# Performance work log

Measured on AMD Instinct MI355X. Metric: run time of the kernel, lower is better.

The kernel has to match this reference:

```python
import jax, jax.numpy as jnp
import numpy as np

B, F, D = 16384, 40, 32

def setup_inputs() -> dict:
    key = jax.random.key(0)
    k1, k2, k3, k4 = jax.random.split(key, 4)
    g = jax.random.uniform(k1, (B, F, F), dtype=jnp.float32)
    h = jax.random.normal(k2, (B, F, D), dtype=jnp.float32)
    # Xavier-normal init for per-field [D,D] weights: std = sqrt(2/(D+D))
    std = float(np.sqrt(2.0 / (D + D)))
    W_in = jax.random.normal(k3, (F, D, D), dtype=jnp.float32) * std
    W_out = jax.random.normal(k4, (F, D, D), dtype=jnp.float32) * std
    bias_p = jnp.zeros((D,), dtype=jnp.float32)
    return {"g": g, "h": h, "W_in": W_in, "W_out": W_out, "bias_p": bias_p}

def reference(g, h, W_in, W_out, bias_p):
    # per-field transform: [F,D,D] x [B,F,D] -> [B,F,D]
    h_out = jnp.einsum('fde,bfe->bfd', W_out, h)
    # graph aggregation over fields: [B,F,F] x [B,F,D] -> [B,F,D]
    aggr = jnp.einsum('bfg,bgd->bfd', g, h_out)
    # per-field transform + bias
    a = jnp.einsum('fde,bfe->bfd', W_in, aggr) + bias_p
    return a
```

## Files before the change

### kernel.cpp

```cpp
#include <hip/hip_runtime.h>


#define B_TOT 16384
#define FF    40
#define DD    32
#define NB    8
#define WF    10

__global__ __launch_bounds__(256, 4)
void graph_layer_fused(const float* __restrict__ g,
                       const float* __restrict__ h,
                       const float* __restrict__ Win,
                       const float* __restrict__ Wout,
                       const float* __restrict__ bias,
                       float* __restrict__ out)
{
    __shared__ __attribute__((aligned(16))) float s_buf[NB * FF * DD];

    const int t     = threadIdx.x;
    const int w     = t >> 6;
    const int l     = t & 63;
    const int b0    = blockIdx.x * NB;
    const int fbase = w * WF;

    {
        const float4* src = (const float4*)(h + (size_t)b0 * (FF * DD));
        float4* dst = (float4*)s_buf;
        #pragma unroll
        for (int k = 0; k < 10; ++k)
            dst[t + k * 256] = src[t + k * 256];
    }
    __syncthreads();

    const int d    = l & 31;
    const int half = l >> 5;
    float accA[WF][4];
    #pragma unroll
    for (int fi = 0; fi < WF; ++fi) {
        const int f = fbase + fi;
        const float4* wrow = (const float4*)(Wout + ((size_t)f * DD + d) * DD);
        float4 wr[8];
        #pragma unroll
        for (int j = 0; j < 8; ++j) wr[j] = wrow[j];
        #pragma unroll
        for (int bp = 0; bp < 4; ++bp) {
            const int bl = 2 * bp + half;
            const float4* hrow = (const float4*)(s_buf + (bl * FF + f) * DD);
            float p0 = 0.f, p1 = 0.f, p2 = 0.f, p3 = 0.f;
            #pragma unroll
            for (int j = 0; j < 8; ++j) {
                float4 hv = hrow[j];
                p0 += wr[j].x * hv.x; p1 += wr[j].y * hv.y;
                p2 += wr[j].z * hv.z; p3 += wr[j].w * hv.w;
            }
            accA[fi][bp] = (p0 + p1) + (p2 + p3);
        }
    }
    __syncthreads();
    #pragma unroll
    for (int fi = 0; fi < WF; ++fi)
        #pragma unroll
        for (int bp = 0; bp < 4; ++bp) {
            const int bl = 2 * bp + half;
            s_buf[(fbase + fi) * (NB * DD) + bl * DD + d] = accA[fi][bp];
        }
    __syncthreads();

    const int bl = l >> 3;
    const int dq = l & 7;
    const float* grow = g + (size_t)(b0 + bl) * (FF * FF) + (size_t)fbase * FF;
    const float* sb   = s_buf + l * 4;

    float4 accB[WF];
    float4 gv[WF];
    #pragma unroll
    for (int fi = 0; fi < WF; ++fi) {
        accB[fi] = make_float4(0.f, 0.f, 0.f, 0.f);
        gv[fi]   = *(const float4*)(grow + fi * FF);
    }
    #pragma unroll 1
    for (int gc = 0; gc < 10; ++gc) {
        float4 hv[4];
        #pragma unroll
        for (int i = 0; i < 4; ++i)
            hv[i] = *(const float4*)(sb + (4 * gc + i) * (NB * DD));
        const int gnx = (gc < 9) ? 4 * gc + 4 : 36;
        #pragma unroll
        for (int fi = 0; fi < WF; ++fi) {
            float4 gf = gv[fi];
            accB[fi].x += gf.x*hv[0].x + gf.y*hv[1].x + gf.z*hv[2].x + gf.w*hv[3].x;
            accB[fi].y += gf.x*hv[0].y + gf.y*hv[1].y + gf.z*hv[2].y + gf.w*hv[3].y;
            accB[fi].z += gf.x*hv[0].z + gf.y*hv[1].z + gf.z*hv[2].z + gf.w*hv[3].z;
            accB[fi].w += gf.x*hv[0].w + gf.y*hv[1].w + gf.z*hv[2].w + gf.w*hv[3].w;
            gv[fi] = *(const float4*)(grow + fi * FF + gnx);
        }
    }
    __syncthreads();
    #pragma unroll
    for (int fi = 0; fi < WF; ++fi)
        *(float4*)(s_buf + (fbase + fi) * (NB * DD) + bl * DD + dq * 4) = accB[fi];
    __syncthreads();

    {
        const float bv = bias[d];
        #pragma unroll
        for (int fi = 0; fi < WF; ++fi) {
            const int f = fbase + fi;
            const float4* wrow = (const float4*)(Win + ((size_t)f * DD + d) * DD);
            float4 wr[8];
            #pragma unroll
            for (int j = 0; j < 8; ++j) wr[j] = wrow[j];
            #pragma unroll
            for (int bp = 0; bp < 4; ++bp) {
                const int bl2 = 2 * bp + half;
                const float4* arow = (const float4*)(s_buf + f * (NB * DD) + bl2 * DD);
                float p0 = 0.f, p1 = 0.f, p2 = 0.f, p3 = 0.f;
                #pragma unroll
                for (int j = 0; j < 8; ++j) {
                    float4 av = arow[j];
                    p0 += wr[j].x * av.x; p1 += wr[j].y * av.y;
                    p2 += wr[j].z * av.z; p3 += wr[j].w * av.w;
                }
                out[((size_t)(b0 + bl2) * FF + f) * DD + d] =
                    ((p0 + p1) + (p2 + p3)) + bv;
            }
        }
    }
}

extern "C" void kernel_launch(void* const* d_in, const int* in_sizes, int n_in,
                              void* d_out, int out_size, void* d_ws, size_t ws_size,
                              hipStream_t stream) {
    const float* g    = (const float*)d_in[0];
    const float* h    = (const float*)d_in[1];
    const float* Win  = (const float*)d_in[2];
    const float* Wout = (const float*)d_in[3];
    const float* bias = (const float*)d_in[4];
    float* out = (float*)d_out;

    dim3 block(256);
    dim3 grid(B_TOT / NB);
    graph_layer_fused<<<grid, block, 0, stream>>>(g, h, Win, Wout, bias, out);
}
```

Baseline: 374.4 us.

## Halve batch tile, write stage results in place, drop barriers

Each block now processes 4 batch rows instead of 8, which halves LDS use and doubles the launch-bounds occupancy target. The per-field transform writes its results back in place in the [b][f][d] layout, so the separate register accumulator and transposed store pass go away along with one barrier. The aggregation stage's thread mapping changes so each wave only produces the fields it later consumes, which lets a per-wave s_waitcnt stand in for the final __syncthreads. The risk is that smaller tiles reload the weights and g rows more often per batch row, and that the correctness now depends on same-wave ordering of LDS accesses.

```diff
diff --git a/kernel.cpp b/kernel.cpp
--- a/kernel.cpp
+++ b/kernel.cpp
@@ -4,10 +4,10 @@
 #define B_TOT 16384
 #define FF    40
 #define DD    32
-#define NB    8
+#define NB    4
 #define WF    10
 
-__global__ __launch_bounds__(256, 4)
+__global__ __launch_bounds__(256, 8)
 void graph_layer_fused(const float* __restrict__ g,
                        const float* __restrict__ h,
                        const float* __restrict__ Win,
@@ -27,15 +27,14 @@
         const float4* src = (const float4*)(h + (size_t)b0 * (FF * DD));
         float4* dst = (float4*)s_buf;
         #pragma unroll
-        for (int k = 0; k < 10; ++k)
+        for (int k = 0; k < 5; ++k)
             dst[t + k * 256] = src[t + k * 256];
     }
     __syncthreads();
 
     const int d    = l & 31;
     const int half = l >> 5;
-    float accA[WF][4];
-    #pragma unroll
+    #pragma unroll 1
     for (int fi = 0; fi < WF; ++fi) {
         const int f = fbase + fi;
         const float4* wrow = (const float4*)(Wout + ((size_t)f * DD + d) * DD);
@@ -43,67 +42,70 @@
         #pragma unroll
         for (int j = 0; j < 8; ++j) wr[j] = wrow[j];
         #pragma unroll
-        for (int bp = 0; bp < 4; ++bp) {
+        for (int bp = 0; bp < 2; ++bp) {
             const int bl = 2 * bp + half;
-            const float4* hrow = (const float4*)(s_buf + (bl * FF + f) * DD);
+            float* row = s_buf + (bl * FF + f) * DD;
             float p0 = 0.f, p1 = 0.f, p2 = 0.f, p3 = 0.f;
             #pragma unroll
             for (int j = 0; j < 8; ++j) {
-                float4 hv = hrow[j];
+                float4 hv = ((const float4*)row)[j];
                 p0 += wr[j].x * hv.x; p1 += wr[j].y * hv.y;
                 p2 += wr[j].z * hv.z; p3 += wr[j].w * hv.w;
             }
-            accA[fi][bp] = (p0 + p1) + (p2 + p3);
+            row[d] = (p0 + p1) + (p2 + p3);
         }
     }
     __syncthreads();
+
+    const int bl = l >> 4;
+    const int dq = (l >> 1) & 7;
+    const int fh = l & 1;
+    const int f0 = fbase + fh * 5;
+    const float* grow = g + (size_t)(b0 + bl) * (FF * FF) + (size_t)f0 * FF;
+    const float* sbB  = s_buf + bl * (FF * DD) + dq * 4;
+
+    float4 accB[5];
+    float4 gv[5];
     #pragma unroll
-    for (int fi = 0; fi < WF; ++fi)
-        #pragma unroll
-        for (int bp = 0; bp < 4; ++bp) {
-            const int bl = 2 * bp + half;
-            s_buf[(fbase + fi) * (NB * DD) + bl * DD + d] = accA[fi][bp];
-        }
-    __syncthreads();
-
-    const int bl = l >> 3;
-    const int dq = l & 7;
-    const float* grow = g + (size_t)(b0 + bl) * (FF * FF) + (size_t)fbase * FF;
-    const float* sb   = s_buf + l * 4;
-
-    float4 accB[WF];
-    float4 gv[WF];
-    #pragma unroll
-    for (int fi = 0; fi < WF; ++fi) {
+    for (int fi = 0; fi < 5; ++fi) {
         accB[fi] = make_float4(0.f, 0.f, 0.f, 0.f);
         gv[fi]   = *(const float4*)(grow + fi * FF);
     }
     #pragma unroll 1
     for (int gc = 0; gc < 10; ++gc) {
-        float4 hv[4];
+        const int gnx = (gc < 9) ? 4 * gc + 4 : 36;
+        float4 h0 = *(const float4*)(sbB + (4 * gc + 0) * DD);
+        float4 h1 = *(const float4*)(sbB + (4 * gc + 1) * DD);
         #pragma unroll
-        for (int i = 0; i < 4; ++i)
-            hv[i] = *(const float4*)(sb + (4 * gc + i) * (NB * DD));
-        const int gnx = (gc < 9) ? 4 * gc + 4 : 36;
+        for (int fi = 0; fi < 5; ++fi) {
+            float4 gf = gv[fi];
+            accB[fi].x += gf.x * h0.x + gf.y * h1.x;
+            accB[fi].y += gf.x * h0.y + gf.y * h1.y;
+            accB[fi].z += gf.x * h0.z + gf.y * h1.z;
+            accB[fi].w += gf.x * h0.w + gf.y * h1.w;
+        }
+        float4 h2 = *(const float4*)(sbB + (4 * gc + 2) * DD);
+        float4 h3 = *(const float4*)(sbB + (4 * gc + 3) * DD);
         #pragma unroll
-        for (int fi = 0; fi < WF; ++fi) {
+        for (int fi = 0; fi < 5; ++fi) {
             float4 gf = gv[fi];
-            accB[fi].x += gf.x*hv[0].x + gf.y*hv[1].x + gf.z*hv[2].x + gf.w*hv[3].x;
-            accB[fi].y += gf.x*hv[0].y + gf.y*hv[1].y + gf.z*hv[2].y + gf.w*hv[3].y;
-            accB[fi].z += gf.x*hv[0].z + gf.y*hv[1].z + gf.z*hv[2].z + gf.w*hv[3].z;
-            accB[fi].w += gf.x*hv[0].w + gf.y*hv[1].w + gf.z*hv[2].w + gf.w*hv[3].w;
+            accB[fi].x += gf.z * h2.x + gf.w * h3.x;
+            accB[fi].y += gf.z * h2.y + gf.w * h3.y;
+            accB[fi].z += gf.z * h2.z + gf.w * h3.z;
+            accB[fi].w += gf.z * h2.w + gf.w * h3.w;
             gv[fi] = *(const float4*)(grow + fi * FF + gnx);
         }
     }
     __syncthreads();
+
     #pragma unroll
-    for (int fi = 0; fi < WF; ++fi)
-        *(float4*)(s_buf + (fbase + fi) * (NB * DD) + bl * DD + dq * 4) = accB[fi];
-    __syncthreads();
+    for (int fi = 0; fi < 5; ++fi)
+        *(float4*)(s_buf + ((size_t)bl * FF + f0 + fi) * DD + dq * 4) = accB[fi];
+    asm volatile("s_waitcnt lgkmcnt(0)" ::: "memory");
 
     {
         const float bv = bias[d];
-        #pragma unroll
+        #pragma unroll 1
         for (int fi = 0; fi < WF; ++fi) {
             const int f = fbase + fi;
             const float4* wrow = (const float4*)(Win + ((size_t)f * DD + d) * DD);
@@ -111,9 +113,9 @@
             #pragma unroll
             for (int j = 0; j < 8; ++j) wr[j] = wrow[j];
             #pragma unroll
-            for (int bp = 0; bp < 4; ++bp) {
+            for (int bp = 0; bp < 2; ++bp) {
                 const int bl2 = 2 * bp + half;
-                const float4* arow = (const float4*)(s_buf + f * (NB * DD) + bl2 * DD);
+                const float4* arow = (const float4*)(s_buf + (bl2 * FF + f) * DD);
                 float p0 = 0.f, p1 = 0.f, p2 = 0.f, p3 = 0.f;
                 #pragma unroll
                 for (int j = 0; j < 8; ++j) {
```

Measured after the change: 524.9 us. +40.2%, slower.
